# Performance work log

Measured on AMD Instinct MI355X. Metric: run time of the kernel, lower is better.

The kernel has to match this reference:

```python
import jax, jax.numpy as jnp
import numpy as np

B, N, C, H, W = 4, 64, 256, 64, 64
ROI = 7          # roi_samples
S = 3            # ceil(16px / 7) sample points per ROI cell (boxes fixed at 16px)
HALF = 0.125     # fixed normalized half-size -> 16px boxes on 64-grid -> static S
N_INT = ROI * S  # interpolation grid side length (21)


def setup_inputs() -> dict:
    key = jax.random.key(0)
    k1, k2, k3, k4, k5 = jax.random.split(key, 5)
    img = jax.random.normal(k1, (B, C, H, W), jnp.float32)
    cen = jax.random.uniform(k2, (B, N, 2), jnp.float32, minval=0.2, maxval=0.8)
    # boxes_bn22 = [(x1,y1),(x2,y2)], normalized coords, fixed size so that
    # custom_roi_align's ceil(box_px/roi) == S for every box
    boxes = jnp.stack([cen - HALF, cen + HALF], axis=2)  # (B,N,2,2)
    conv_w = jax.random.normal(k3, (C, C, ROI, ROI), jnp.float32) * 0.02
    conv_b = jnp.zeros((C,), jnp.float32)
    cxcywh_w = jax.random.normal(k4, (C, 4), jnp.float32) * 0.02
    cxcywh_b = jnp.zeros((C,), jnp.float32)
    posenc_w = jax.random.normal(k5, (C, C + 2), jnp.float32) * 0.02
    posenc_b = jnp.zeros((C,), jnp.float32)
    return {"image_tokens_bchw": img, "boxes_bn22": boxes,
            "conv_w": conv_w, "conv_b": conv_b,
            "cxcywh_w": cxcywh_w, "cxcywh_b": cxcywh_b,
            "posenc_w": posenc_w, "posenc_b": posenc_b}


def _pe_1d(coord, num_feats):
    # DETR/SAM-style sinusoidal PE of a scalar coordinate -> (n, num_feats)
    dim_t = 10000.0 ** (2.0 * (jnp.arange(num_feats) // 2) / num_feats)
    pos = coord[:, None] * (2.0 * jnp.pi) / dim_t.astype(coord.dtype)
    enc = jnp.stack([jnp.sin(pos[:, 0::2]), jnp.cos(pos[:, 1::2])], axis=-1)
    return enc.reshape(coord.shape[0], num_feats)


def _roi_align(img_bchw, boxes_f4, bidx):
    # Faithful vectorization of custom_roi_align: per-box uniform sample grid,
    # bilinear grid_sample (align_corners=True, border pad), then SxS avg-pool.
    nsx = W / (W - 1.0)
    nsy = H / (H - 1.0)
    t = jnp.arange(N_INT, dtype=img_bchw.dtype) / (N_INT - 1)

    def one(b, box):
        x1, y1, x2, y2 = box[0] * nsx, box[1] * nsy, box[2] * nsx, box[3] * nsy
        hsx = (x2 - x1) / (2 * N_INT)
        hsy = (y2 - y1) / (2 * N_INT)
        gx = (x1 + hsx) + t * (x2 - x1 - 2 * hsx)  # linspace over box interior
        gy = (y1 + hsy) + t * (y2 - y1 - 2 * hsy)
        # align_corners=True pixel coords; border padding == clamp
        px = jnp.clip(gx * (W - 1), 0.0, W - 1.0)
        py = jnp.clip(gy * (H - 1), 0.0, H - 1.0)
        x0f, y0f = jnp.floor(px), jnp.floor(py)
        wx, wy = px - x0f, py - y0f
        x0 = jnp.clip(x0f.astype(jnp.int32), 0, W - 1)
        x1i = jnp.clip(x0 + 1, 0, W - 1)
        y0 = jnp.clip(y0f.astype(jnp.int32), 0, H - 1)
        y1i = jnp.clip(y0 + 1, 0, H - 1)
        img = img_bchw[b]                               # (C,H,W)
        v00 = img[:, y0[:, None], x0[None, :]]          # (C,N_INT,N_INT)
        v01 = img[:, y0[:, None], x1i[None, :]]
        v10 = img[:, y1i[:, None], x0[None, :]]
        v11 = img[:, y1i[:, None], x1i[None, :]]
        top = v00 + (v01 - v00) * wx[None, None, :]
        bot = v10 + (v11 - v10) * wx[None, None, :]
        samp = top + (bot - top) * wy[None, :, None]    # (C,N_INT,N_INT)
        # avg_pool2d with kernel (S,S) stride (S,S)
        return samp.reshape(C, ROI, S, ROI, S).mean(axis=(2, 4))  # (C,ROI,ROI)

    return jax.vmap(one)(bidx, boxes_f4)


def reference(image_tokens_bchw, boxes_bn22, conv_w, conv_b,
              cxcywh_w, cxcywh_b, posenc_w, posenc_b):
    boxes_f4 = boxes_bn22.reshape(B * N, 4)
    bidx = jnp.repeat(jnp.arange(B), N)
    roi = _roi_align(image_tokens_bchw, boxes_f4, bidx)      # (BN,C,ROI,ROI)
    # 7x7 conv over a 7x7 map -> 1x1: a plain contraction
    img_enc = (jnp.einsum('nchw,ochw->no', roi, conv_w) + conv_b).reshape(B, N, C)

    cen = boxes_bn22.mean(axis=2)                            # (B,N,2) cx,cy
    wh = boxes_bn22[:, :, 1] - boxes_bn22[:, :, 0]           # (B,N,2) w,h
    cxcywh = jnp.concatenate([cen, wh], axis=-1)             # (B,N,4)
    flat = cxcywh.reshape(B * N, 4)
    x_enc = _pe_1d(flat[:, 0], C // 2)
    y_enc = _pe_1d(flat[:, 1], C // 2)
    pe_tok = jnp.concatenate([y_enc, x_enc, flat[:, 3:4], flat[:, 2:3]], axis=-1)
    pos_enc = (pe_tok @ posenc_w.T + posenc_b).reshape(B, N, C)
    base = cxcywh @ cxcywh_w.T + cxcywh_b                    # (B,N,C)
    return base + pos_enc + img_enc
```

## Files before the change

kernel.cpp:

```cpp
#include <hip/hip_runtime.h>

static constexpr int KDIM = 12544;
static constexpr float TWO_PI = 6.28318530717958647692f;

typedef float f32x4 __attribute__((ext_vector_type(4)));
typedef short bf16x8 __attribute__((ext_vector_type(8)));

__device__ inline float bf2f(unsigned short u) {
    union { unsigned int i; float f; } x; x.i = ((unsigned int)u) << 16; return x.f;
}
__device__ inline unsigned short f2bf(float f) {
    union { float f; unsigned int i; } x; x.f = f;
    unsigned int r = (x.i + 0x7FFFu + ((x.i >> 16) & 1u)) >> 16;
    return (unsigned short)r;
}

__global__ __launch_bounds__(256) void k_small(
    const float* __restrict__ boxes,
    const float* __restrict__ cxw, const float* __restrict__ cxb,
    const float* __restrict__ pw,  const float* __restrict__ pb,
    const float* __restrict__ cb,
    float* __restrict__ out,
    float4* __restrict__ lutx, float4* __restrict__ luty)
{
    const int n   = blockIdx.x;
    const int tid = threadIdx.x;

    const float bx1 = boxes[n*4+0], by1 = boxes[n*4+1];
    const float bx2 = boxes[n*4+2], by2 = boxes[n*4+3];
    const float cx = 0.5f*(bx1+bx2), cy = 0.5f*(by1+by2);
    const float wx = bx2-bx1,        wy = by2-by1;

    __shared__ float pe[258];

    if (tid < 128) {
        const int   k     = tid & 63;
        const float coord = (tid < 64) ? cy : cx;
        const float d   = exp2f((float)k * (13.287712379549449f / 64.0f));
        const float arg = coord * TWO_PI / d;
        float s, c;
        sincosf(arg, &s, &c);
        const int base = (tid < 64) ? 0 : 128;
        pe[base + 2*k]     = s;
        pe[base + 2*k + 1] = c;
    } else if (tid == 128) {
        pe[256] = wy;
        pe[257] = wx;
    } else if (tid >= 160 && tid < 202) {
        const int  t   = tid - 160;
        const bool isx = (t < 21);
        const int  i   = isx ? t : (t - 21);
        const float ns = 64.0f / 63.0f;
        const float a1 = (isx ? bx1 : by1) * ns;
        const float a2 = (isx ? bx2 : by2) * ns;
        const float hs = (a2 - a1) * (1.0f / 42.0f);
        const float tt = (float)i * (1.0f / 20.0f);
        const float g  = a1 + hs + tt * (a2 - a1 - 2.0f*hs);
        float p = g * 63.0f;
        p = fminf(fmaxf(p, 0.0f), 63.0f);
        const float p0 = floorf(p);
        const float w  = p - p0;
        int i0 = (int)p0; i0 = min(i0, 63);
        const int i1 = min(i0 + 1, 63);
        (isx ? lutx : luty)[n*21 + i] = make_float4((float)i0, (float)i1, w, 0.0f);
    }
    __syncthreads();

    const int o = tid;
    float acc = pb[o] + cb[o] + cxb[o];
    acc = fmaf(cxw[o*4+0], cx, acc);
    acc = fmaf(cxw[o*4+1], cy, acc);
    acc = fmaf(cxw[o*4+2], wx, acc);
    acc = fmaf(cxw[o*4+3], wy, acc);
    const float* __restrict__ pwr = pw + o*258;
    for (int k = 0; k < 258; ++k)
        acc = fmaf(pe[k], pwr[k], acc);
    out[n*256 + o] = acc;
}

__global__ __launch_bounds__(256) void k_tr(
    const float* __restrict__ img, unsigned short* __restrict__ imgT)
{
    __shared__ float t[64][65];
    const int b  = blockIdx.z;
    const int c0 = blockIdx.x * 64;
    const int p0 = blockIdx.y * 64;
    const int tid = threadIdx.x;
    const int col = tid & 63;
    const int r4  = tid >> 6;
    #pragma unroll
    for (int i = 0; i < 16; ++i) {
        const int row = i*4 + r4;
        t[row][col] = img[((size_t)(b*256 + c0 + row)) * 4096 + p0 + col];
    }
    __syncthreads();
    #pragma unroll
    for (int i = 0; i < 16; ++i) {
        const int prow = i*4 + r4;
        imgT[((size_t)(b*4096 + p0 + prow)) * 256 + c0 + col] = f2bf(t[col][prow]);
    }
}

__global__ __launch_bounds__(256) void k_wt(
    const float* __restrict__ cw, unsigned short* __restrict__ Wt)
{
    __shared__ float t[12544];
    const int o = blockIdx.x, tid = threadIdx.x;
    #pragma unroll
    for (int i = 0; i < 49; ++i)
        t[i*256 + tid] = cw[(size_t)o*12544 + i*256 + tid];
    __syncthreads();
    for (int ij = 0; ij < 49; ++ij)
        Wt[(size_t)o*12544 + ij*256 + tid] = f2bf(t[tid*49 + ij]);
}

__global__ __launch_bounds__(256) void k_roi2(
    const unsigned short* __restrict__ imgT,
    const float4* __restrict__ lutx, const float4* __restrict__ luty,
    unsigned short* __restrict__ A)
{
    const int cell = blockIdx.x * 4 + (threadIdx.x >> 6);
    const int l    = threadIdx.x & 63;
    const int n    = cell / 49;
    const int ij   = cell - n * 49;
    const int pi   = ij / 7;
    const int pj   = ij - pi * 7;
    const int b    = n >> 6;
    const int c4   = l * 4;

    const unsigned short* __restrict__ base = imgT + ((size_t)b << 20) + c4;

    const float4 lx0 = lutx[n*21 + pj*3 + 0];
    const float4 lx1 = lutx[n*21 + pj*3 + 1];
    const float4 lx2 = lutx[n*21 + pj*3 + 2];

    float a0 = 0.f, a1 = 0.f, a2 = 0.f, a3 = 0.f;

    #pragma unroll
    for (int si = 0; si < 3; ++si) {
        const float4 ly = luty[n*21 + pi*3 + si];
        const unsigned short* __restrict__ r0 = base + (((int)ly.x) << 14);
        const unsigned short* __restrict__ r1 = base + (((int)ly.y) << 14);
        const float wyy = ly.z;
        const float4 lxs[3] = {lx0, lx1, lx2};
        #pragma unroll
        for (int sj = 0; sj < 3; ++sj) {
            const float4 lx = lxs[sj];
            const int x0 = ((int)lx.x) << 8, x1 = ((int)lx.y) << 8;
            const float wxx = lx.z;
            const ushort4 v00 = *(const ushort4*)(r0 + x0);
            const ushort4 v01 = *(const ushort4*)(r0 + x1);
            const ushort4 v10 = *(const ushort4*)(r1 + x0);
            const ushort4 v11 = *(const ushort4*)(r1 + x1);
            {
                const float t = fmaf(bf2f(v01.x) - bf2f(v00.x), wxx, bf2f(v00.x));
                const float u = fmaf(bf2f(v11.x) - bf2f(v10.x), wxx, bf2f(v10.x));
                a0 += fmaf(u - t, wyy, t);
            }
            {
                const float t = fmaf(bf2f(v01.y) - bf2f(v00.y), wxx, bf2f(v00.y));
                const float u = fmaf(bf2f(v11.y) - bf2f(v10.y), wxx, bf2f(v10.y));
                a1 += fmaf(u - t, wyy, t);
            }
            {
                const float t = fmaf(bf2f(v01.z) - bf2f(v00.z), wxx, bf2f(v00.z));
                const float u = fmaf(bf2f(v11.z) - bf2f(v10.z), wxx, bf2f(v10.z));
                a2 += fmaf(u - t, wyy, t);
            }
            {
                const float t = fmaf(bf2f(v01.w) - bf2f(v00.w), wxx, bf2f(v00.w));
                const float u = fmaf(bf2f(v11.w) - bf2f(v10.w), wxx, bf2f(v10.w));
                a3 += fmaf(u - t, wyy, t);
            }
        }
    }
    const float s = 1.0f / 9.0f;
    ushort4 o4;
    o4.x = f2bf(a0 * s); o4.y = f2bf(a1 * s); o4.z = f2bf(a2 * s); o4.w = f2bf(a3 * s);
    *(ushort4*)(A + (size_t)n*KDIM + ij*256 + c4) = o4;
}

__global__ __launch_bounds__(256) void k_gemm_mfma(
    const unsigned short* __restrict__ A, const unsigned short* __restrict__ Wt,
    float* __restrict__ out)
{
    __shared__ __align__(16) char lds[65536];
    const int m0 = blockIdx.x * 64;
    const int o0 = blockIdx.y * 64;
    const int kb = blockIdx.z * 256;
    const int tid = threadIdx.x;

    #pragma unroll
    for (int it = 0; it < 8; ++it) {
        const int chunk = tid + it * 256;
        const int row = chunk >> 5;
        const int ci  = chunk & 31;
        const int lb  = (row * 512 + ci * 16) ^ ((row & 7) << 4);
        *(float4*)&lds[lb] =
            *(const float4*)(A  + (size_t)(m0 + row) * KDIM + kb + ci * 8);
        *(float4*)&lds[32768 + lb] =
            *(const float4*)(Wt + (size_t)(o0 + row) * KDIM + kb + ci * 8);
    }
    __syncthreads();

    const int w   = tid >> 6;
    const int l   = tid & 63;
    const int l15 = l & 15;
    const int lg  = l >> 4;

    f32x4 acc[4] = {};

    const int bcol = w * 16 + l15;
    const int brow512 = bcol * 512;
    const int bxor    = (bcol & 7) << 4;
    #pragma unroll
    for (int ks = 0; ks < 8; ++ks) {
        const int koff = ks * 64 + lg * 16;
        const bf16x8 bfrag = *(const bf16x8*)&lds[32768 + ((brow512 + koff) ^ bxor)];
        #pragma unroll
        for (int mi = 0; mi < 4; ++mi) {
            const int arow = mi * 16 + l15;
            const bf16x8 afrag =
                *(const bf16x8*)&lds[(arow * 512 + koff) ^ ((arow & 7) << 4)];
            acc[mi] = __builtin_amdgcn_mfma_f32_16x16x32_bf16(afrag, bfrag, acc[mi], 0, 0, 0);
        }
    }

    #pragma unroll
    for (int mi = 0; mi < 4; ++mi)
        #pragma unroll
        for (int j = 0; j < 4; ++j) {
            const int m = m0 + mi * 16 + lg * 4 + j;
            const int o = o0 + w * 16 + l15;
            unsafeAtomicAdd(&out[m * 256 + o], acc[mi][j]);
        }
}

extern "C" void kernel_launch(void* const* d_in, const int* in_sizes, int n_in,
                              void* d_out, int out_size, void* d_ws, size_t ws_size,
                              hipStream_t stream)
{
    const float* img   = (const float*)d_in[0];
    const float* boxes = (const float*)d_in[1];
    const float* convw = (const float*)d_in[2];
    const float* convb = (const float*)d_in[3];
    const float* cxw   = (const float*)d_in[4];
    const float* cxb   = (const float*)d_in[5];
    const float* pw    = (const float*)d_in[6];
    const float* pb    = (const float*)d_in[7];
    float* out = (float*)d_out;

    unsigned short* imgT = (unsigned short*)d_ws;
    unsigned short* Wt   = (unsigned short*)d_ws;
    unsigned short* A    = (unsigned short*)((char*)d_ws + 8388608);
    float4* lutx = (float4*)((char*)d_ws + 14811136);
    float4* luty = (float4*)((char*)d_ws + 14897152);

    k_small<<<256, 256, 0, stream>>>(boxes, cxw, cxb, pw, pb, convb, out, lutx, luty);
    k_tr<<<dim3(4, 64, 4), 256, 0, stream>>>(img, imgT);
    k_roi2<<<3136, 256, 0, stream>>>(imgT, lutx, luty, A);
    k_wt<<<256, 256, 0, stream>>>(convw, Wt);
    k_gemm_mfma<<<dim3(4, 4, 49), 256, 0, stream>>>(A, Wt, out);
}
```

Baseline: 137.4 us.

## Fuse ROI sampling into GEMM, merge prep kernels, replace atomics with partial reduce

Merges the box/PE, image transpose and weight transpose kernels into one launch dispatched by block index. ROI bilinear sampling now writes directly into LDS inside the MFMA GEMM kernel, one block per (32 boxes, ROI cell), which removes the A matrix round trip through global memory. Split-K atomics are replaced by per-cell partial buffers summed in a separate reduce kernel. The fused kernel launches only 392 blocks and loops over four output chunks, and the partial buffer adds about 12.8MB of writes and reads.

```diff
diff --git a/kernel.cpp b/kernel.cpp
--- a/kernel.cpp
+++ b/kernel.cpp
@@ -15,225 +15,223 @@
     return (unsigned short)r;
 }
 
-__global__ __launch_bounds__(256) void k_small(
+__global__ __launch_bounds__(256) void k_prep(
     const float* __restrict__ boxes,
     const float* __restrict__ cxw, const float* __restrict__ cxb,
     const float* __restrict__ pw,  const float* __restrict__ pb,
     const float* __restrict__ cb,
+    const float* __restrict__ img, const float* __restrict__ convw,
     float* __restrict__ out,
+    unsigned short* __restrict__ imgT, unsigned short* __restrict__ Wt,
     float4* __restrict__ lutx, float4* __restrict__ luty)
 {
-    const int n   = blockIdx.x;
+    __shared__ float smem[12544];
+    const int bid = blockIdx.x;
     const int tid = threadIdx.x;
 
-    const float bx1 = boxes[n*4+0], by1 = boxes[n*4+1];
-    const float bx2 = boxes[n*4+2], by2 = boxes[n*4+3];
-    const float cx = 0.5f*(bx1+bx2), cy = 0.5f*(by1+by2);
-    const float wx = bx2-bx1,        wy = by2-by1;
-
-    __shared__ float pe[258];
-
-    if (tid < 128) {
-        const int   k     = tid & 63;
-        const float coord = (tid < 64) ? cy : cx;
-        const float d   = exp2f((float)k * (13.287712379549449f / 64.0f));
-        const float arg = coord * TWO_PI / d;
-        float s, c;
-        sincosf(arg, &s, &c);
-        const int base = (tid < 64) ? 0 : 128;
-        pe[base + 2*k]     = s;
-        pe[base + 2*k + 1] = c;
-    } else if (tid == 128) {
-        pe[256] = wy;
-        pe[257] = wx;
-    } else if (tid >= 160 && tid < 202) {
-        const int  t   = tid - 160;
-        const bool isx = (t < 21);
-        const int  i   = isx ? t : (t - 21);
-        const float ns = 64.0f / 63.0f;
-        const float a1 = (isx ? bx1 : by1) * ns;
-        const float a2 = (isx ? bx2 : by2) * ns;
-        const float hs = (a2 - a1) * (1.0f / 42.0f);
-        const float tt = (float)i * (1.0f / 20.0f);
-        const float g  = a1 + hs + tt * (a2 - a1 - 2.0f*hs);
-        float p = g * 63.0f;
-        p = fminf(fmaxf(p, 0.0f), 63.0f);
-        const float p0 = floorf(p);
-        const float w  = p - p0;
-        int i0 = (int)p0; i0 = min(i0, 63);
-        const int i1 = min(i0 + 1, 63);
-        (isx ? lutx : luty)[n*21 + i] = make_float4((float)i0, (float)i1, w, 0.0f);
+    if (bid < 256) {
+        const int n = bid;
+        const float bx1 = boxes[n*4+0], by1 = boxes[n*4+1];
+        const float bx2 = boxes[n*4+2], by2 = boxes[n*4+3];
+        const float cx = 0.5f*(bx1+bx2), cy = 0.5f*(by1+by2);
+        const float wx = bx2-bx1,        wy = by2-by1;
+
+        float* pe = smem;
+
+        if (tid < 128) {
+            const int   k     = tid & 63;
+            const float coord = (tid < 64) ? cy : cx;
+            const float d   = exp2f((float)k * (13.287712379549449f / 64.0f));
+            const float arg = coord * TWO_PI / d;
+            float s, c;
+            sincosf(arg, &s, &c);
+            const int base = (tid < 64) ? 0 : 128;
+            pe[base + 2*k]     = s;
+            pe[base + 2*k + 1] = c;
+        } else if (tid == 128) {
+            pe[256] = wy;
+            pe[257] = wx;
+        } else if (tid >= 160 && tid < 202) {
+            const int  t   = tid - 160;
+            const bool isx = (t < 21);
+            const int  i   = isx ? t : (t - 21);
+            const float ns = 64.0f / 63.0f;
+            const float a1 = (isx ? bx1 : by1) * ns;
+            const float a2 = (isx ? bx2 : by2) * ns;
+            const float hs = (a2 - a1) * (1.0f / 42.0f);
+            const float tt = (float)i * (1.0f / 20.0f);
+            const float g  = a1 + hs + tt * (a2 - a1 - 2.0f*hs);
+            float p = g * 63.0f;
+            p = fminf(fmaxf(p, 0.0f), 63.0f);
+            const float p0 = floorf(p);
+            const float w  = p - p0;
+            int i0 = (int)p0; i0 = min(i0, 63);
+            const int i1 = min(i0 + 1, 63);
+            (isx ? lutx : luty)[n*21 + i] = make_float4((float)i0, (float)i1, w, 0.0f);
+        }
+        __syncthreads();
+
+        const int o = tid;
+        float acc = pb[o] + cb[o] + cxb[o];
+        acc = fmaf(cxw[o*4+0], cx, acc);
+        acc = fmaf(cxw[o*4+1], cy, acc);
+        acc = fmaf(cxw[o*4+2], wx, acc);
+        acc = fmaf(cxw[o*4+3], wy, acc);
+        const float* __restrict__ pwr = pw + o*258;
+        for (int k = 0; k < 258; ++k)
+            acc = fmaf(pe[k], pwr[k], acc);
+        out[n*256 + o] = acc;
+    } else if (bid < 1280) {
+        float (*t)[65] = (float(*)[65])smem;
+        const int idx = bid - 256;
+        const int b   = idx >> 8;
+        const int rem = idx & 255;
+        const int c0  = (rem & 3) * 64;
+        const int p0  = (rem >> 2) * 64;
+        const int col = tid & 63;
+        const int r4  = tid >> 6;
+        #pragma unroll
+        for (int i = 0; i < 16; ++i) {
+            const int row = i*4 + r4;
+            t[row][col] = img[((size_t)(b*256 + c0 + row)) * 4096 + p0 + col];
+        }
+        __syncthreads();
+        #pragma unroll
+        for (int i = 0; i < 16; ++i) {
+            const int prow = i*4 + r4;
+            imgT[((size_t)(b*4096 + p0 + prow)) * 256 + c0 + col] = f2bf(t[col][prow]);
+        }
+    } else {
+        const int o = bid - 1280;
+        #pragma unroll
+        for (int i = 0; i < 49; ++i)
+            smem[i*256 + tid] = convw[(size_t)o*12544 + i*256 + tid];
+        __syncthreads();
+        for (int ij = 0; ij < 49; ++ij)
+            Wt[(size_t)o*12544 + ij*256 + tid] = f2bf(smem[tid*49 + ij]);
+    }
+}
+
+__global__ __launch_bounds__(256) void k_fused(
+    const unsigned short* __restrict__ imgT,
+    const unsigned short* __restrict__ Wt,
+    const float4* __restrict__ lutx, const float4* __restrict__ luty,
+    float* __restrict__ partial)
+{
+    __shared__ __align__(16) char ldsA[16384];
+    __shared__ __align__(16) char ldsW[32768];
+
+    const int mt = blockIdx.x;
+    const int ij = blockIdx.y;
+    const int m0 = mt * 32;
+    const int pi = ij / 7, pj = ij - pi * 7;
+    const int tid = threadIdx.x;
+    const int w = tid >> 6, l = tid & 63;
+    const int l15 = l & 15, lg = l >> 4;
+    const int c4 = l * 4;
+
+    for (int bi = 0; bi < 8; ++bi) {
+        const int r = w * 8 + bi;
+        const int n = m0 + r;
+        const int b = n >> 6;
+        const unsigned short* __restrict__ base = imgT + ((size_t)b << 20) + c4;
+
+        const float4 lx0 = lutx[n*21 + pj*3 + 0];
+        const float4 lx1 = lutx[n*21 + pj*3 + 1];
+        const float4 lx2 = lutx[n*21 + pj*3 + 2];
+
+        float a0 = 0.f, a1 = 0.f, a2 = 0.f, a3 = 0.f;
+        #pragma unroll
+        for (int si = 0; si < 3; ++si) {
+            const float4 ly = luty[n*21 + pi*3 + si];
+            const unsigned short* __restrict__ r0 = base + (((int)ly.x) << 14);
+            const unsigned short* __restrict__ r1 = base + (((int)ly.y) << 14);
+            const float wyy = ly.z;
+            const float4 lxs[3] = {lx0, lx1, lx2};
+            #pragma unroll
+            for (int sj = 0; sj < 3; ++sj) {
+                const float4 lx = lxs[sj];
+                const int x0 = ((int)lx.x) << 8, x1 = ((int)lx.y) << 8;
+                const float wxx = lx.z;
+                const ushort4 v00 = *(const ushort4*)(r0 + x0);
+                const ushort4 v01 = *(const ushort4*)(r0 + x1);
+                const ushort4 v10 = *(const ushort4*)(r1 + x0);
+                const ushort4 v11 = *(const ushort4*)(r1 + x1);
+                {
+                    const float t = fmaf(bf2f(v01.x) - bf2f(v00.x), wxx, bf2f(v00.x));
+                    const float u = fmaf(bf2f(v11.x) - bf2f(v10.x), wxx, bf2f(v10.x));
+                    a0 += fmaf(u - t, wyy, t);
+                }
+                {
+                    const float t = fmaf(bf2f(v01.y) - bf2f(v00.y), wxx, bf2f(v00.y));
+                    const float u = fmaf(bf2f(v11.y) - bf2f(v10.y), wxx, bf2f(v10.y));
+                    a1 += fmaf(u - t, wyy, t);
+                }
+                {
+                    const float t = fmaf(bf2f(v01.z) - bf2f(v00.z), wxx, bf2f(v00.z));
+                    const float u = fmaf(bf2f(v11.z) - bf2f(v10.z), wxx, bf2f(v10.z));
+                    a2 += fmaf(u - t, wyy, t);
+                }
+                {
+                    const float t = fmaf(bf2f(v01.w) - bf2f(v00.w), wxx, bf2f(v00.w));
+                    const float u = fmaf(bf2f(v11.w) - bf2f(v10.w), wxx, bf2f(v10.w));
+                    a3 += fmaf(u - t, wyy, t);
+                }
+            }
+        }
+        const float s = 1.0f / 9.0f;
+        ushort4 o4;
+        o4.x = f2bf(a0 * s); o4.y = f2bf(a1 * s);
+        o4.z = f2bf(a2 * s); o4.w = f2bf(a3 * s);
+        *(ushort4*)&ldsA[(r * 512 + l * 8) ^ ((r & 7) << 4)] = o4;
     }
     __syncthreads();
 
-    const int o = tid;
-    float acc = pb[o] + cb[o] + cxb[o];
-    acc = fmaf(cxw[o*4+0], cx, acc);
-    acc = fmaf(cxw[o*4+1], cy, acc);
-    acc = fmaf(cxw[o*4+2], wx, acc);
-    acc = fmaf(cxw[o*4+3], wy, acc);
-    const float* __restrict__ pwr = pw + o*258;
-    for (int k = 0; k < 258; ++k)
-        acc = fmaf(pe[k], pwr[k], acc);
-    out[n*256 + o] = acc;
-}
-
-__global__ __launch_bounds__(256) void k_tr(
-    const float* __restrict__ img, unsigned short* __restrict__ imgT)
-{
-    __shared__ float t[64][65];
-    const int b  = blockIdx.z;
-    const int c0 = blockIdx.x * 64;
-    const int p0 = blockIdx.y * 64;
-    const int tid = threadIdx.x;
-    const int col = tid & 63;
-    const int r4  = tid >> 6;
+    float* __restrict__ pp = partial + (size_t)ij * 65536;
+    const int bcol = w * 16 + l15;
+    #pragma unroll 1
+    for (int oc = 0; oc < 4; ++oc) {
+        if (oc) __syncthreads();
+        #pragma unroll
+        for (int it = 0; it < 8; ++it) {
+            const int chunk = tid + it * 256;
+            const int row = chunk >> 5, ci = chunk & 31;
+            *(float4*)&ldsW[(row * 512 + ci * 16) ^ ((row & 7) << 4)] =
+                *(const float4*)(Wt + (size_t)(oc * 64 + row) * KDIM + ij * 256 + ci * 8);
+        }
+        __syncthreads();
+
+        f32x4 acc[2] = {};
+        #pragma unroll
+        for (int ks = 0; ks < 8; ++ks) {
+            const int koff = ks * 64 + lg * 16;
+            const bf16x8 bfrag =
+                *(const bf16x8*)&ldsW[(bcol * 512 + koff) ^ ((bcol & 7) << 4)];
+            #pragma unroll
+            for (int mi = 0; mi < 2; ++mi) {
+                const int arow = mi * 16 + l15;
+                const bf16x8 afrag =
+                    *(const bf16x8*)&ldsA[(arow * 512 + koff) ^ ((arow & 7) << 4)];
+                acc[mi] = __builtin_amdgcn_mfma_f32_16x16x32_bf16(afrag, bfrag, acc[mi], 0, 0, 0);
+            }
+        }
+        #pragma unroll
+        for (int mi = 0; mi < 2; ++mi)
+            #pragma unroll
+            for (int j = 0; j < 4; ++j)
+                pp[(m0 + mi * 16 + lg * 4 + j) * 256 + oc * 64 + bcol] = acc[mi][j];
+    }
+}
+
+__global__ __launch_bounds__(256) void k_reduce(
+    const float* __restrict__ partial, float* __restrict__ out)
+{
+    const int e = blockIdx.x * 256 + threadIdx.x;
+    float s = out[e];
     #pragma unroll
-    for (int i = 0; i < 16; ++i) {
-        const int row = i*4 + r4;
-        t[row][col] = img[((size_t)(b*256 + c0 + row)) * 4096 + p0 + col];
-    }
-    __syncthreads();
-    #pragma unroll
-    for (int i = 0; i < 16; ++i) {
-        const int prow = i*4 + r4;
-        imgT[((size_t)(b*4096 + p0 + prow)) * 256 + c0 + col] = f2bf(t[col][prow]);
-    }
-}
-
-__global__ __launch_bounds__(256) void k_wt(
-    const float* __restrict__ cw, unsigned short* __restrict__ Wt)
-{
-    __shared__ float t[12544];
-    const int o = blockIdx.x, tid = threadIdx.x;
-    #pragma unroll
-    for (int i = 0; i < 49; ++i)
-        t[i*256 + tid] = cw[(size_t)o*12544 + i*256 + tid];
-    __syncthreads();
     for (int ij = 0; ij < 49; ++ij)
-        Wt[(size_t)o*12544 + ij*256 + tid] = f2bf(t[tid*49 + ij]);
-}
-
-__global__ __launch_bounds__(256) void k_roi2(
-    const unsigned short* __restrict__ imgT,
-    const float4* __restrict__ lutx, const float4* __restrict__ luty,
-    unsigned short* __restrict__ A)
-{
-    const int cell = blockIdx.x * 4 + (threadIdx.x >> 6);
-    const int l    = threadIdx.x & 63;
-    const int n    = cell / 49;
-    const int ij   = cell - n * 49;
-    const int pi   = ij / 7;
-    const int pj   = ij - pi * 7;
-    const int b    = n >> 6;
-    const int c4   = l * 4;
-
-    const unsigned short* __restrict__ base = imgT + ((size_t)b << 20) + c4;
-
-    const float4 lx0 = lutx[n*21 + pj*3 + 0];
-    const float4 lx1 = lutx[n*21 + pj*3 + 1];
-    const float4 lx2 = lutx[n*21 + pj*3 + 2];
-
-    float a0 = 0.f, a1 = 0.f, a2 = 0.f, a3 = 0.f;
-
-    #pragma unroll
-    for (int si = 0; si < 3; ++si) {
-        const float4 ly = luty[n*21 + pi*3 + si];
-        const unsigned short* __restrict__ r0 = base + (((int)ly.x) << 14);
-        const unsigned short* __restrict__ r1 = base + (((int)ly.y) << 14);
-        const float wyy = ly.z;
-        const float4 lxs[3] = {lx0, lx1, lx2};
-        #pragma unroll
-        for (int sj = 0; sj < 3; ++sj) {
-            const float4 lx = lxs[sj];
-            const int x0 = ((int)lx.x) << 8, x1 = ((int)lx.y) << 8;
-            const float wxx = lx.z;
-            const ushort4 v00 = *(const ushort4*)(r0 + x0);
-            const ushort4 v01 = *(const ushort4*)(r0 + x1);
-            const ushort4 v10 = *(const ushort4*)(r1 + x0);
-            const ushort4 v11 = *(const ushort4*)(r1 + x1);
-            {
-                const float t = fmaf(bf2f(v01.x) - bf2f(v00.x), wxx, bf2f(v00.x));
-                const float u = fmaf(bf2f(v11.x) - bf2f(v10.x), wxx, bf2f(v10.x));
-                a0 += fmaf(u - t, wyy, t);
-            }
-            {
-                const float t = fmaf(bf2f(v01.y) - bf2f(v00.y), wxx, bf2f(v00.y));
-                const float u = fmaf(bf2f(v11.y) - bf2f(v10.y), wxx, bf2f(v10.y));
-                a1 += fmaf(u - t, wyy, t);
-            }
-            {
-                const float t = fmaf(bf2f(v01.z) - bf2f(v00.z), wxx, bf2f(v00.z));
-                const float u = fmaf(bf2f(v11.z) - bf2f(v10.z), wxx, bf2f(v10.z));
-                a2 += fmaf(u - t, wyy, t);
-            }
-            {
-                const float t = fmaf(bf2f(v01.w) - bf2f(v00.w), wxx, bf2f(v00.w));
-                const float u = fmaf(bf2f(v11.w) - bf2f(v10.w), wxx, bf2f(v10.w));
-                a3 += fmaf(u - t, wyy, t);
-            }
-        }
-    }
-    const float s = 1.0f / 9.0f;
-    ushort4 o4;
-    o4.x = f2bf(a0 * s); o4.y = f2bf(a1 * s); o4.z = f2bf(a2 * s); o4.w = f2bf(a3 * s);
-    *(ushort4*)(A + (size_t)n*KDIM + ij*256 + c4) = o4;
-}
-
-__global__ __launch_bounds__(256) void k_gemm_mfma(
-    const unsigned short* __restrict__ A, const unsigned short* __restrict__ Wt,
-    float* __restrict__ out)
-{
-    __shared__ __align__(16) char lds[65536];
-    const int m0 = blockIdx.x * 64;
-    const int o0 = blockIdx.y * 64;
-    const int kb = blockIdx.z * 256;
-    const int tid = threadIdx.x;
-
-    #pragma unroll
-    for (int it = 0; it < 8; ++it) {
-        const int chunk = tid + it * 256;
-        const int row = chunk >> 5;
-        const int ci  = chunk & 31;
-        const int lb  = (row * 512 + ci * 16) ^ ((row & 7) << 4);
-        *(float4*)&lds[lb] =
-            *(const float4*)(A  + (size_t)(m0 + row) * KDIM + kb + ci * 8);
-        *(float4*)&lds[32768 + lb] =
-            *(const float4*)(Wt + (size_t)(o0 + row) * KDIM + kb + ci * 8);
-    }
-    __syncthreads();
-
-    const int w   = tid >> 6;
-    const int l   = tid & 63;
-    const int l15 = l & 15;
-    const int lg  = l >> 4;
-
-    f32x4 acc[4] = {};
-
-    const int bcol = w * 16 + l15;
-    const int brow512 = bcol * 512;
-    const int bxor    = (bcol & 7) << 4;
-    #pragma unroll
-    for (int ks = 0; ks < 8; ++ks) {
-        const int koff = ks * 64 + lg * 16;
-        const bf16x8 bfrag = *(const bf16x8*)&lds[32768 + ((brow512 + koff) ^ bxor)];
-        #pragma unroll
-        for (int mi = 0; mi < 4; ++mi) {
-            const int arow = mi * 16 + l15;
-            const bf16x8 afrag =
-                *(const bf16x8*)&lds[(arow * 512 + koff) ^ ((arow & 7) << 4)];
-            acc[mi] = __builtin_amdgcn_mfma_f32_16x16x32_bf16(afrag, bfrag, acc[mi], 0, 0, 0);
-        }
-    }
-
-    #pragma unroll
-    for (int mi = 0; mi < 4; ++mi)
-        #pragma unroll
-        for (int j = 0; j < 4; ++j) {
-            const int m = m0 + mi * 16 + lg * 4 + j;
-            const int o = o0 + w * 16 + l15;
-            unsafeAtomicAdd(&out[m * 256 + o], acc[mi][j]);
-        }
+        s += partial[(size_t)ij * 65536 + e];
+    out[e] = s;
 }
 
 extern "C" void kernel_launch(void* const* d_in, const int* in_sizes, int n_in,
@@ -250,15 +248,14 @@
     const float* pb    = (const float*)d_in[7];
     float* out = (float*)d_out;
 
-    unsigned short* imgT = (unsigned short*)d_ws;
-    unsigned short* Wt   = (unsigned short*)d_ws;
-    unsigned short* A    = (unsigned short*)((char*)d_ws + 8388608);
-    float4* lutx = (float4*)((char*)d_ws + 14811136);
-    float4* luty = (float4*)((char*)d_ws + 14897152);
-
-    k_small<<<256, 256, 0, stream>>>(boxes, cxw, cxb, pw, pb, convb, out, lutx, luty);
-    k_tr<<<dim3(4, 64, 4), 256, 0, stream>>>(img, imgT);
-    k_roi2<<<3136, 256, 0, stream>>>(imgT, lutx, luty, A);
-    k_wt<<<256, 256, 0, stream>>>(convw, Wt);
-    k_gemm_mfma<<<dim3(4, 4, 49), 256, 0, stream>>>(A, Wt, out);
-}
+    unsigned short* imgT    = (unsigned short*)d_ws;
+    unsigned short* Wt      = (unsigned short*)((char*)d_ws + 8388608);
+    float*          partial = (float*)((char*)d_ws + 14811136);
+    float4*         lutx    = (float4*)((char*)d_ws + 27656192);
+    float4*         luty    = (float4*)((char*)d_ws + 27742208);
+
+    k_prep<<<1536, 256, 0, stream>>>(boxes, cxw, cxb, pw, pb, convb,
+                                     img, convw, out, imgT, Wt, lutx, luty);
+    k_fused<<<dim3(8, 49), 256, 0, stream>>>(imgT, Wt, lutx, luty, partial);
+    k_reduce<<<256, 256, 0, stream>>>(partial, out);
+}
```

After: 131.9 us. 4.1% less time.
